# Optimization experiments

Hardware: AMD Instinct MI355X
Metric: run time of the kernel (lower is better)

Reference implementation:

```python
import jax, jax.numpy as jnp
import numpy as np

B, S, H = 1, 2048, 2048
NH, HD, RD = 32, 64, 64      # n_heads, head_dim, qk_mqa_dim (rope dim)
QR, KVR = 1024, 896          # q_lora_rank, kv_lora_rank
EPS = 1e-6
SCALE = HD ** -0.5           # scaling = head_dim ** -0.5 (as in module)


def rotate_half(x):
    x1, x2 = jnp.split(x, 2, axis=-1)
    return jnp.concatenate((-x2, x1), axis=-1)


def rmsnorm(x, w):
    var = jnp.mean(jnp.square(x), axis=-1, keepdims=True)
    return x * jax.lax.rsqrt(var + EPS) * w


def setup_inputs() -> dict:
    key = jax.random.key(0)
    ks = jax.random.split(key, 8)
    hidden_states = jax.random.normal(ks[0], (B, S, H), jnp.float32)
    # rotary tables over RD dims (applied only to the rope slice)
    inv_freq = 1.0 / (10000.0 ** (np.arange(0, RD, 2, dtype=np.float32) / RD))
    ang = np.arange(S, dtype=np.float32)[:, None] * inv_freq[None, :]
    emb = np.concatenate([ang, ang], axis=-1)  # [S, RD]
    cos = jnp.tile(jnp.asarray(np.cos(emb))[None], (B, 1, 1))
    sin = jnp.tile(jnp.asarray(np.sin(emb))[None], (B, 1, 1))
    s = 0.02
    q_a_w = s * jax.random.normal(ks[1], (QR, H), jnp.float32)
    q_a_ln_w = jnp.ones((QR,), jnp.float32)
    q_b_w = s * jax.random.normal(ks[2], (NH * (HD + RD), QR), jnp.float32)
    kv_a_w = s * jax.random.normal(ks[3], (KVR + RD, H), jnp.float32)
    kv_a_ln_w = jnp.ones((KVR,), jnp.float32)
    kv_b_w = s * jax.random.normal(ks[4], (NH * 2 * HD, KVR), jnp.float32)
    o_w = s * jax.random.normal(ks[5], (H, NH * HD), jnp.float32)
    return {"hidden_states": hidden_states, "cos": cos, "sin": sin,
            "q_a_w": q_a_w, "q_a_ln_w": q_a_ln_w, "q_b_w": q_b_w,
            "kv_a_w": kv_a_w, "kv_a_ln_w": kv_a_ln_w, "kv_b_w": kv_b_w,
            "o_w": o_w}


def reference(hidden_states, cos, sin, q_a_w, q_a_ln_w, q_b_w,
              kv_a_w, kv_a_ln_w, kv_b_w, o_w):
    b, s, _ = hidden_states.shape
    # Q: low-rank down -> RMSNorm -> up, split nope/rope per head
    q_lat = rmsnorm(hidden_states @ q_a_w.T, q_a_ln_w)             # [B,S,QR]
    q = (q_lat @ q_b_w.T).reshape(b, s, NH, HD + RD).transpose(0, 2, 1, 3)
    q_nope, q_rope = q[..., :HD], q[..., HD:]                      # [B,NH,S,HD/RD]
    # KV: joint down-proj with shared MQA rope key
    ckv = hidden_states @ kv_a_w.T                                 # [B,S,KVR+RD]
    c_kv, k_rope = ckv[..., :KVR], ckv[..., KVR:]
    k_rope = k_rope[:, None]                                       # [B,1,S,RD]
    kv = (rmsnorm(c_kv, kv_a_ln_w) @ kv_b_w.T).reshape(b, s, NH, 2 * HD)
    kv = kv.transpose(0, 2, 1, 3)                                  # [B,NH,S,2HD]
    k_nope, v = kv[..., :HD], kv[..., HD:]
    # RoPE on rope slices only (cos/sin unsqueezed over head dim)
    c_, s_ = cos[:, None], sin[:, None]
    q_rope = q_rope * c_ + rotate_half(q_rope) * s_
    k_rope = k_rope * c_ + rotate_half(k_rope) * s_
    q_full = jnp.concatenate([q_nope, q_rope], axis=-1)            # [B,NH,S,HD+RD]
    k_full = jnp.concatenate(
        [k_nope, jnp.broadcast_to(k_rope, (b, NH, s, RD))], axis=-1)
    # causal SDPA
    scores = jnp.einsum('bhqd,bhkd->bhqk', q_full, k_full) * SCALE
    mask = jnp.tril(jnp.ones((s, s), bool))
    scores = jnp.where(mask, scores, jnp.finfo(scores.dtype).min)
    attn = jax.nn.softmax(scores, axis=-1)
    out = jnp.einsum('bhqk,bhkd->bhqd', attn, v)                   # [B,NH,S,HD]
    out = out.transpose(0, 2, 1, 3).reshape(b, s, NH * HD)
    return out @ o_w.T                                             # [B,S,H]
```

## Files before the change

### kernel.cpp

```cpp
#include <hip/hip_runtime.h>


typedef __attribute__((ext_vector_type(8))) __bf16 bf16x8;
typedef __attribute__((ext_vector_type(4))) float f32x4;
typedef __attribute__((ext_vector_type(4))) unsigned u32x4;

__device__ __forceinline__ unsigned short f2bf(float f) {
  unsigned int x = __builtin_bit_cast(unsigned int, f);
  x += 0x7fffu + ((x >> 16) & 1u);
  return (unsigned short)(x >> 16);
}
__device__ __forceinline__ void gload_lds16(const void* g, void* l) {
  __builtin_amdgcn_global_load_lds(
      (const __attribute__((address_space(1))) void*)g,
      (__attribute__((address_space(3))) void*)l, 16, 0, 0);
}

struct CvtSegs {
  const float* src[6];
  unsigned short* dst[6];
  unsigned int n_src[6];
  unsigned int n_tot[6];
  unsigned int blk0[7];
};

__global__ __launch_bounds__(256) void cvt_all(CvtSegs sg) {
  int b = blockIdx.x;
  int seg = 0;
#pragma unroll
  for (int k = 0; k < 5; ++k)
    if (b >= (int)sg.blk0[k + 1]) seg = k + 1;
  size_t i = ((size_t)(b - sg.blk0[seg]) * 256 + threadIdx.x) * 4;
  if (i >= sg.n_tot[seg]) return;
  unsigned short o0 = 0, o1 = 0, o2 = 0, o3 = 0;
  if (i < sg.n_src[seg]) {
    float4 v = *reinterpret_cast<const float4*>(sg.src[seg] + i);
    o0 = f2bf(v.x); o1 = f2bf(v.y); o2 = f2bf(v.z); o3 = f2bf(v.w);
  }
  *reinterpret_cast<ushort4*>(sg.dst[seg] + i) = make_ushort4(o0, o1, o2, o3);
}

__global__ __launch_bounds__(512, 4) void gemm_bt2(const unsigned short* __restrict__ A,
                                                   const unsigned short* __restrict__ B,
                                                   float* __restrict__ C,
                                                   int M, int N, int K) {
  __shared__ unsigned short lA0[128 * 64], lA1[128 * 64];
  __shared__ unsigned short lB0[64 * 64], lB1[64 * 64];
  const int tid = threadIdx.x, lane = tid & 63, wv = tid >> 6;
  const int wr = wv >> 1, wc = wv & 1;
  const int bm = blockIdx.y * 128, bn = blockIdx.x * 64;

  f32x4 acc[2][2] = {};

  const int ar0 = tid >> 3;
  const int acol = (((tid & 7) ^ ((tid >> 3) & 7))) * 8;
  const int swz = lane & 7;

  auto stage = [&](unsigned short* la, unsigned short* lb, int k0) {
#pragma unroll
    for (int i = 0; i < 2; ++i)
      gload_lds16(A + (size_t)(bm + i * 64 + ar0) * K + k0 + acol,
                  &la[(i * 512 + wv * 64) * 8]);
    gload_lds16(B + (size_t)(bn + ar0) * K + k0 + acol, &lb[(wv * 64) * 8]);
  };

  auto compute = [&](const unsigned short* la, const unsigned short* lb) {
#pragma unroll
    for (int ks = 0; ks < 2; ++ks) {
      const int ch = ((ks * 4 + (lane >> 4)) ^ swz) * 8;
      bf16x8 af[2], bfr[2];
#pragma unroll
      for (int m = 0; m < 2; ++m)
        af[m] = *reinterpret_cast<const bf16x8*>(
            &la[(wr * 32 + m * 16 + (lane & 15)) * 64 + ch]);
#pragma unroll
      for (int n = 0; n < 2; ++n)
        bfr[n] = *reinterpret_cast<const bf16x8*>(
            &lb[(wc * 32 + n * 16 + (lane & 15)) * 64 + ch]);
      __builtin_amdgcn_s_setprio(1);
#pragma unroll
      for (int m = 0; m < 2; ++m)
#pragma unroll
        for (int n = 0; n < 2; ++n)
          acc[m][n] = __builtin_amdgcn_mfma_f32_16x16x32_bf16(af[m], bfr[n], acc[m][n], 0, 0, 0);
      __builtin_amdgcn_s_setprio(0);
    }
  };

  stage(lA0, lB0, 0);
  for (int k0 = 0; k0 < K; k0 += 128) {
    __syncthreads();
    stage(lA1, lB1, k0 + 64);
    compute(lA0, lB0);
    __syncthreads();
    if (k0 + 128 < K) stage(lA0, lB0, k0 + 128);
    compute(lA1, lB1);
  }

  const int r0 = bm + wr * 32, c0 = bn + wc * 32;
#pragma unroll
  for (int m = 0; m < 2; ++m)
#pragma unroll
    for (int n = 0; n < 2; ++n)
#pragma unroll
      for (int r = 0; r < 4; ++r)
        C[(size_t)(r0 + m * 16 + (lane >> 4) * 4 + r) * N + c0 + n * 16 + (lane & 15)] =
            acc[m][n][r];
}

__global__ __launch_bounds__(256) void rmsnorm_rope(const float* __restrict__ C1,
                                                    const float* __restrict__ qw,
                                                    const float* __restrict__ kvw,
                                                    const float* __restrict__ cosp,
                                                    const float* __restrict__ sinp,
                                                    unsigned short* __restrict__ qn,
                                                    unsigned short* __restrict__ ckvn,
                                                    unsigned short* __restrict__ kr) {
  const int s = blockIdx.x, tid = threadIdx.x;
  const float* row = C1 + (size_t)s * 2048;
  __shared__ float red[4];

  float4 v = *reinterpret_cast<const float4*>(row + tid * 4);
  float ss = v.x * v.x + v.y * v.y + v.z * v.z + v.w * v.w;
  ss += __shfl_xor(ss, 32); ss += __shfl_xor(ss, 16); ss += __shfl_xor(ss, 8);
  ss += __shfl_xor(ss, 4);  ss += __shfl_xor(ss, 2);  ss += __shfl_xor(ss, 1);
  if ((tid & 63) == 0) red[tid >> 6] = ss;
  __syncthreads();
  float rs = rsqrtf((red[0] + red[1] + red[2] + red[3]) * (1.f / 1024.f) + 1e-6f);
  {
    float4 w = *reinterpret_cast<const float4*>(qw + tid * 4);
    *reinterpret_cast<ushort4*>(qn + (size_t)s * 1024 + tid * 4) =
        make_ushort4(f2bf(v.x * rs * w.x), f2bf(v.y * rs * w.y),
                     f2bf(v.z * rs * w.z), f2bf(v.w * rs * w.w));
  }

  float4 u = make_float4(0.f, 0.f, 0.f, 0.f);
  if (tid < 224) u = *reinterpret_cast<const float4*>(row + 1024 + tid * 4);
  ss = u.x * u.x + u.y * u.y + u.z * u.z + u.w * u.w;
  ss += __shfl_xor(ss, 32); ss += __shfl_xor(ss, 16); ss += __shfl_xor(ss, 8);
  ss += __shfl_xor(ss, 4);  ss += __shfl_xor(ss, 2);  ss += __shfl_xor(ss, 1);
  __syncthreads();
  if ((tid & 63) == 0) red[tid >> 6] = ss;
  __syncthreads();
  rs = rsqrtf((red[0] + red[1] + red[2] + red[3]) * (1.f / 896.f) + 1e-6f);
  if (tid < 224) {
    float4 w = *reinterpret_cast<const float4*>(kvw + tid * 4);
    *reinterpret_cast<ushort4*>(ckvn + (size_t)s * 896 + tid * 4) =
        make_ushort4(f2bf(u.x * rs * w.x), f2bf(u.y * rs * w.y),
                     f2bf(u.z * rs * w.z), f2bf(u.w * rs * w.w));
  }

  if (tid < 64) {
    int d = tid;
    float x = row[1920 + d];
    float part = (d < 32) ? -row[1920 + d + 32] : row[1920 + d - 32];
    float vv = x * cosp[(size_t)s * 64 + d] + part * sinp[(size_t)s * 64 + d];
    kr[(size_t)s * 64 + d] = f2bf(vv);
  }
}

__global__ __launch_bounds__(256) void q_post(const float* __restrict__ Qf,
                                              const float* __restrict__ cosp,
                                              const float* __restrict__ sinp,
                                              unsigned short* __restrict__ Qb) {
  size_t base = ((size_t)blockIdx.x * 256 + threadIdx.x) * 4;
  int s = (int)(base >> 12);
  int w = (int)(base & 127);
  float4 x = *reinterpret_cast<const float4*>(Qf + base);
  float4 o;
  if (w < 64) {
    o = x;
  } else {
    int d = w - 64;
    float sgn = (d < 32) ? -1.f : 1.f;
    float4 prt = (d < 32) ? *reinterpret_cast<const float4*>(Qf + base + 32)
                          : *reinterpret_cast<const float4*>(Qf + base - 32);
    float4 c = *reinterpret_cast<const float4*>(cosp + (size_t)s * 64 + d);
    float4 sn = *reinterpret_cast<const float4*>(sinp + (size_t)s * 64 + d);
    o.x = x.x * c.x + sgn * prt.x * sn.x;
    o.y = x.y * c.y + sgn * prt.y * sn.y;
    o.z = x.z * c.z + sgn * prt.z * sn.z;
    o.w = x.w * c.w + sgn * prt.w * sn.w;
  }
  const float SC = 0.18033688f;
  *reinterpret_cast<ushort4*>(Qb + base) =
      make_ushort4(f2bf(o.x * SC), f2bf(o.y * SC), f2bf(o.z * SC), f2bf(o.w * SC));
}

__global__ __launch_bounds__(256) void kv_post(const float* __restrict__ KVf,
                                               const unsigned short* __restrict__ kr,
                                               unsigned short* __restrict__ Kb,
                                               unsigned short* __restrict__ Vt) {
  __shared__ float lT[64 * 65];
  const int s0 = blockIdx.x * 64, h = blockIdx.y, tid = threadIdx.x;
  for (int idx = tid; idx < 4096; idx += 256) {
    int r = idx >> 6, c = idx & 63;
    size_t base = (size_t)(s0 + r) * 4096 + h * 128;
    Kb[base + c] = f2bf(KVf[base + c]);
    Kb[base + 64 + c] = kr[(size_t)(s0 + r) * 64 + c];
    lT[r * 65 + c] = KVf[base + 64 + c];
  }
  __syncthreads();
  for (int idx = tid; idx < 4096; idx += 256) {
    int d = idx >> 6, c = idx & 63;
    Vt[((size_t)h * 64 + d) * 2048 + s0 + c] = f2bf(lT[c * 65 + d]);
  }
}

__global__ __launch_bounds__(256, 4) void flash_attn(const unsigned short* __restrict__ Qb,
                                                     const unsigned short* __restrict__ Kb,
                                                     const unsigned short* __restrict__ Vt,
                                                     float* __restrict__ Op,
                                                     float2* __restrict__ Ml) {
  __shared__ unsigned short lK0[64 * 128], lK1[64 * 128];
  const int tid = threadIdx.x, lane = tid & 63, wv = tid >> 6;
  const int h = blockIdx.x;
  const int qb = 31 - ((int)blockIdx.y >> 1);
  const int j = (int)blockIdx.y & 1;
  const int q0 = qb * 64;
  const int firstrow = q0 + wv * 16;
  const int qa = firstrow + (lane & 15);

  bf16x8 qf[4];
  {
    const unsigned short* qrow = Qb + (size_t)(firstrow + (lane & 15)) * 4096 + h * 128;
#pragma unroll
    for (int ks = 0; ks < 4; ++ks)
      qf[ks] = *reinterpret_cast<const bf16x8*>(qrow + ks * 32 + (lane >> 4) * 8);
  }

  f32x4 o_acc[4] = {};
  float mrow = -1e30f, lrow = 0.f;

  const int g = lane >> 4;
  const int sl0 = ((g & 1) * 2) * 16 + (lane & 15);
  const int sl1 = sl0 + 16;
  const bool hi = g >= 2;

  const int krow = wv * 4 + (lane >> 4);
  const int kcol = (((lane & 15) ^ (krow & 7)) * 8);
  const int swz = lane & 7;

  auto stage = [&](int t, unsigned short* lK) {
    int j0 = t * 64;
#pragma unroll
    for (int i = 0; i < 4; ++i)
      gload_lds16(Kb + (size_t)(j0 + i * 16 + krow) * 4096 + h * 128 + kcol,
                  &lK[(i * 16 + wv * 4) * 128]);
  };

  auto loadV = [&](int j0, bf16x8 (&vr)[2][4]) {
#pragma unroll
    for (int ks = 0; ks < 2; ++ks)
#pragma unroll
      for (int n = 0; n < 4; ++n)
        vr[ks][n] = *reinterpret_cast<const bf16x8*>(
            Vt + ((size_t)h * 64 + n * 16 + (lane & 15)) * 2048 + j0 + ks * 32 +
            (lane >> 4) * 8);
  };

  auto computeT = [&](int j0, const unsigned short* lK, const bf16x8 (&vr)[2][4]) {
    f32x4 sT[4] = {};
    __builtin_amdgcn_s_setprio(1);
#pragma unroll
    for (int n = 0; n < 4; ++n)
#pragma unroll
      for (int ks = 0; ks < 4; ++ks) {
        bf16x8 kf = *reinterpret_cast<const bf16x8*>(
            &lK[(n * 16 + (lane & 15)) * 128 + (((ks * 4 + (lane >> 4)) ^ swz)) * 8]);
        sT[n] = __builtin_amdgcn_mfma_f32_16x16x32_bf16(kf, qf[ks], sT[n], 0, 0, 0);
      }
    __builtin_amdgcn_s_setprio(0);

    if (j0 == q0) {
#pragma unroll
      for (int n = 0; n < 4; ++n)
#pragma unroll
        for (int r = 0; r < 4; ++r) {
          int key = j0 + n * 16 + g * 4 + r;
          if (key > qa) sT[n][r] = -1e30f;
        }
    }

    float mx = sT[0][0];
#pragma unroll
    for (int n = 0; n < 4; ++n)
#pragma unroll
      for (int r = 0; r < 4; ++r) mx = fmaxf(mx, sT[n][r]);
    mx = fmaxf(mx, __shfl_xor(mx, 16));
    mx = fmaxf(mx, __shfl_xor(mx, 32));

    if (__any(mx - mrow > 8.0f)) {
      float mn = fmaxf(mrow, mx);
      float sf = exp2f(mrow - mn);
      mrow = mn;
      lrow *= sf;
      float sfr[4];
#pragma unroll
      for (int r = 0; r < 4; ++r) sfr[r] = __shfl(sf, (lane >> 4) * 4 + r);
#pragma unroll
      for (int n = 0; n < 4; ++n)
#pragma unroll
        for (int r = 0; r < 4; ++r) o_acc[n][r] *= sfr[r];
    }

    float ps = 0.f;
    unsigned dw[4][2];
#pragma unroll
    for (int n = 0; n < 4; ++n) {
      float p0 = exp2f(sT[n][0] - mrow), p1 = exp2f(sT[n][1] - mrow);
      float p2 = exp2f(sT[n][2] - mrow), p3 = exp2f(sT[n][3] - mrow);
      ps += (p0 + p1) + (p2 + p3);
      asm("v_cvt_pk_bf16_f32 %0, %1, %2" : "=v"(dw[n][0]) : "v"(p0), "v"(p1));
      asm("v_cvt_pk_bf16_f32 %0, %1, %2" : "=v"(dw[n][1]) : "v"(p2), "v"(p3));
    }
    ps += __shfl_xor(ps, 16);
    ps += __shfl_xor(ps, 32);
    lrow += ps;

#pragma unroll
    for (int ks = 0; ks < 2; ++ks) {
      unsigned A0 = __shfl(dw[2 * ks][0], sl0);
      unsigned B0 = __shfl(dw[2 * ks + 1][0], sl0);
      unsigned A1 = __shfl(dw[2 * ks][1], sl0);
      unsigned B1 = __shfl(dw[2 * ks + 1][1], sl0);
      unsigned A2 = __shfl(dw[2 * ks][0], sl1);
      unsigned B2 = __shfl(dw[2 * ks + 1][0], sl1);
      unsigned A3 = __shfl(dw[2 * ks][1], sl1);
      unsigned B3 = __shfl(dw[2 * ks + 1][1], sl1);
      u32x4 mm;
      mm.x = hi ? B0 : A0; mm.y = hi ? B1 : A1;
      mm.z = hi ? B2 : A2; mm.w = hi ? B3 : A3;
      bf16x8 pa = __builtin_bit_cast(bf16x8, mm);
      __builtin_amdgcn_s_setprio(1);
#pragma unroll
      for (int n = 0; n < 4; ++n)
        o_acc[n] = __builtin_amdgcn_mfma_f32_16x16x32_bf16(pa, vr[ks][n], o_acc[n], 0, 0, 0);
      __builtin_amdgcn_s_setprio(0);
    }
  };

  bf16x8 vr[2][4];
  unsigned short* cur = lK0;
  unsigned short* nxt = lK1;
  if (j <= qb) stage(j, cur);
  for (int t = j; t <= qb; t += 2) {
    __syncthreads();
    if (t + 2 <= qb) stage(t + 2, nxt);
    loadV(t * 64, vr);
    computeT(t * 64, cur, vr);
    unsigned short* tmp = cur; cur = nxt; nxt = tmp;
  }

  float* op = Op + (size_t)j * 4194304 + ((size_t)h * 2048 + firstrow) * 64;
#pragma unroll
  for (int n = 0; n < 4; ++n)
#pragma unroll
    for (int r = 0; r < 4; ++r)
      op[(size_t)(g * 4 + r) * 64 + n * 16 + (lane & 15)] = o_acc[n][r];
  if (lane < 16)
    Ml[(size_t)j * 65536 + h * 2048 + qa] = make_float2(mrow, lrow);
}

__global__ __launch_bounds__(256) void flash_combine(const float* __restrict__ Op,
                                                     const float2* __restrict__ Ml,
                                                     unsigned short* __restrict__ Ao) {
  size_t i4 = ((size_t)blockIdx.x * 256 + threadIdx.x) * 4;
  int s = (int)(i4 >> 11);
  int c = (int)(i4 & 2047);
  int h = c >> 6, d = c & 63;
  float2 a = Ml[h * 2048 + s];
  float2 b = Ml[65536 + h * 2048 + s];
  float M = fmaxf(a.x, b.x);
  float w0 = exp2f(a.x - M), w1 = exp2f(b.x - M);
  float inv = 1.f / (w0 * a.y + w1 * b.y);
  size_t pidx = ((size_t)h * 2048 + s) * 64 + d;
  float4 o0 = *reinterpret_cast<const float4*>(Op + pidx);
  float4 o1 = *reinterpret_cast<const float4*>(Op + 4194304 + pidx);
  *reinterpret_cast<ushort4*>(Ao + (size_t)s * 2048 + h * 64 + d) =
      make_ushort4(f2bf((w0 * o0.x + w1 * o1.x) * inv),
                   f2bf((w0 * o0.y + w1 * o1.y) * inv),
                   f2bf((w0 * o0.z + w1 * o1.z) * inv),
                   f2bf((w0 * o0.w + w1 * o1.w) * inv));
}

extern "C" void kernel_launch(void* const* d_in, const int* in_sizes, int n_in,
                              void* d_out, int out_size, void* d_ws, size_t ws_size,
                              hipStream_t stream) {
  const float* hs   = (const float*)d_in[0];
  const float* cosp = (const float*)d_in[1];
  const float* sinp = (const float*)d_in[2];
  const float* qaw  = (const float*)d_in[3];
  const float* qaln = (const float*)d_in[4];
  const float* qbwf = (const float*)d_in[5];
  const float* kvaw = (const float*)d_in[6];
  const float* kvln = (const float*)d_in[7];
  const float* kvbwf= (const float*)d_in[8];
  const float* owf  = (const float*)d_in[9];
  float* out = (float*)d_out;
  char* ws = (char*)d_ws;
  const size_t MB = 1u << 20;

  unsigned short* W1b  = (unsigned short*)(ws + 0);
  unsigned short* Ao   = (unsigned short*)(ws + 0);
  unsigned short* qbw  = (unsigned short*)(ws + 8 * MB);
  unsigned short* Vt   = (unsigned short*)(ws + 8 * MB);
  unsigned short* kvbw = (unsigned short*)(ws + 16 * MB);
  unsigned short* owb  = (unsigned short*)(ws + 23 * MB);
  unsigned short* hsb  = (unsigned short*)(ws + 31 * MB);
  unsigned short* Qb   = (unsigned short*)(ws + 31 * MB);
  float*          C1   = (float*)(ws + 39 * MB);
  unsigned short* Kb   = (unsigned short*)(ws + 47 * MB);
  unsigned short* qln  = (unsigned short*)(ws + 55 * MB);
  unsigned short* ckvn = (unsigned short*)(ws + 59 * MB);
  unsigned short* kr   = (unsigned short*)(ws + 63 * MB);
  float*          Qf   = (float*)(ws + 64 * MB);
  float*          KVf  = (float*)(ws + 96 * MB);
  float*          Op   = (float*)(ws + 64 * MB);
  float2*         Mlp  = (float2*)(ws + 98 * MB);
  (void)ws_size; (void)in_sizes; (void)n_in; (void)out_size;

  CvtSegs sg;
  sg.src[0] = qaw;   sg.dst[0] = W1b;                      sg.n_src[0] = 1024u * 2048u; sg.n_tot[0] = 1024u * 2048u;
  sg.src[1] = kvaw;  sg.dst[1] = W1b + (size_t)1024 * 2048; sg.n_src[1] = 960u * 2048u;  sg.n_tot[1] = 1024u * 2048u;
  sg.src[2] = hs;    sg.dst[2] = hsb;                      sg.n_src[2] = 2048u * 2048u; sg.n_tot[2] = 2048u * 2048u;
  sg.src[3] = qbwf;  sg.dst[3] = qbw;                      sg.n_src[3] = 4096u * 1024u; sg.n_tot[3] = 4096u * 1024u;
  sg.src[4] = kvbwf; sg.dst[4] = kvbw;                     sg.n_src[4] = 4096u * 896u;  sg.n_tot[4] = 4096u * 896u;
  sg.src[5] = owf;   sg.dst[5] = owb;                      sg.n_src[5] = 2048u * 2048u; sg.n_tot[5] = 2048u * 2048u;
  sg.blk0[0] = 0;
  for (int k = 0; k < 6; ++k) sg.blk0[k + 1] = sg.blk0[k] + sg.n_tot[k] / 1024u;
  cvt_all<<<dim3(sg.blk0[6]), 256, 0, stream>>>(sg);

  gemm_bt2<<<dim3(32, 16), 512, 0, stream>>>(hsb, W1b, C1, 2048, 2048, 2048);
  rmsnorm_rope<<<2048, 256, 0, stream>>>(C1, qaln, kvln, cosp, sinp, qln, ckvn, kr);
  gemm_bt2<<<dim3(64, 16), 512, 0, stream>>>(qln, qbw, Qf, 2048, 4096, 1024);
  gemm_bt2<<<dim3(64, 16), 512, 0, stream>>>(ckvn, kvbw, KVf, 2048, 4096, 896);

  q_post<<<dim3((unsigned)(((size_t)2048 * 4096) / 1024)), 256, 0, stream>>>(Qf, cosp, sinp, Qb);
  kv_post<<<dim3(32, 32), 256, 0, stream>>>(KVf, kr, Kb, Vt);

  flash_attn<<<dim3(32, 64), 256, 0, stream>>>(Qb, Kb, Vt, Op, Mlp);
  flash_combine<<<dim3(4096), 256, 0, stream>>>(Op, Mlp, Ao);

  gemm_bt2<<<dim3(32, 16), 512, 0, stream>>>(Ao, owb, out, 2048, 2048, 2048);
}
```

Before: 223.3 us.

## Fuse Q RoPE/scale and K assembly into attention, emit bf16 GEMM outputs

The Q and KV up-projection GEMMs now write bf16 directly instead of fp32. The q_post kernel is removed: RoPE and the softmax scale are applied to Q inside flash_attn while fragments load. K tiles are staged straight from the KV GEMM output and the shared rope key buffer, which removes the separate Kb assembly. The GEMM also gets an XCD-aware workgroup index swizzle, and the softmax max/sum reductions are tree-shaped. The intent is to cut intermediate memory traffic and kernel launches. In exchange, Q is rounded to bf16 before RoPE, adding one extra rounding step.

```diff
diff --git a/kernel.cpp b/kernel.cpp
--- a/kernel.cpp
+++ b/kernel.cpp
@@ -10,11 +10,17 @@
   x += 0x7fffu + ((x >> 16) & 1u);
   return (unsigned short)(x >> 16);
 }
+__device__ __forceinline__ float bf2f(unsigned short u) {
+  unsigned int x = ((unsigned int)u) << 16;
+  return __builtin_bit_cast(float, x);
+}
 __device__ __forceinline__ void gload_lds16(const void* g, void* l) {
   __builtin_amdgcn_global_load_lds(
       (const __attribute__((address_space(1))) void*)g,
       (__attribute__((address_space(3))) void*)l, 16, 0, 0);
 }
+__device__ __forceinline__ void cstore(float* C, size_t i, float v) { C[i] = v; }
+__device__ __forceinline__ void cstore(unsigned short* C, size_t i, float v) { C[i] = f2bf(v); }
 
 struct CvtSegs {
   const float* src[6];
@@ -40,15 +46,21 @@
   *reinterpret_cast<ushort4*>(sg.dst[seg] + i) = make_ushort4(o0, o1, o2, o3);
 }
 
+template <typename OutT>
 __global__ __launch_bounds__(512, 4) void gemm_bt2(const unsigned short* __restrict__ A,
                                                    const unsigned short* __restrict__ B,
-                                                   float* __restrict__ C,
+                                                   OutT* __restrict__ C,
                                                    int M, int N, int K) {
   __shared__ unsigned short lA0[128 * 64], lA1[128 * 64];
   __shared__ unsigned short lB0[64 * 64], lB1[64 * 64];
   const int tid = threadIdx.x, lane = tid & 63, wv = tid >> 6;
   const int wr = wv >> 1, wc = wv & 1;
-  const int bm = blockIdx.y * 128, bn = blockIdx.x * 64;
+
+  unsigned nwg = gridDim.x * gridDim.y;
+  unsigned lid = blockIdx.y * gridDim.x + blockIdx.x;
+  unsigned swz_id = (lid & 7) * (nwg >> 3) + (lid >> 3);
+  const int bm = (int)(swz_id / gridDim.x) * 128;
+  const int bn = (int)(swz_id % gridDim.x) * 64;
 
   f32x4 acc[2][2] = {};
 
@@ -104,8 +116,8 @@
     for (int n = 0; n < 2; ++n)
 #pragma unroll
       for (int r = 0; r < 4; ++r)
-        C[(size_t)(r0 + m * 16 + (lane >> 4) * 4 + r) * N + c0 + n * 16 + (lane & 15)] =
-            acc[m][n][r];
+        cstore(C, (size_t)(r0 + m * 16 + (lane >> 4) * 4 + r) * N + c0 + n * 16 + (lane & 15),
+               acc[m][n][r]);
 }
 
 __global__ __launch_bounds__(256) void rmsnorm_rope(const float* __restrict__ C1,
@@ -159,56 +171,26 @@
   }
 }
 
-__global__ __launch_bounds__(256) void q_post(const float* __restrict__ Qf,
-                                              const float* __restrict__ cosp,
-                                              const float* __restrict__ sinp,
-                                              unsigned short* __restrict__ Qb) {
-  size_t base = ((size_t)blockIdx.x * 256 + threadIdx.x) * 4;
-  int s = (int)(base >> 12);
-  int w = (int)(base & 127);
-  float4 x = *reinterpret_cast<const float4*>(Qf + base);
-  float4 o;
-  if (w < 64) {
-    o = x;
-  } else {
-    int d = w - 64;
-    float sgn = (d < 32) ? -1.f : 1.f;
-    float4 prt = (d < 32) ? *reinterpret_cast<const float4*>(Qf + base + 32)
-                          : *reinterpret_cast<const float4*>(Qf + base - 32);
-    float4 c = *reinterpret_cast<const float4*>(cosp + (size_t)s * 64 + d);
-    float4 sn = *reinterpret_cast<const float4*>(sinp + (size_t)s * 64 + d);
-    o.x = x.x * c.x + sgn * prt.x * sn.x;
-    o.y = x.y * c.y + sgn * prt.y * sn.y;
-    o.z = x.z * c.z + sgn * prt.z * sn.z;
-    o.w = x.w * c.w + sgn * prt.w * sn.w;
-  }
-  const float SC = 0.18033688f;
-  *reinterpret_cast<ushort4*>(Qb + base) =
-      make_ushort4(f2bf(o.x * SC), f2bf(o.y * SC), f2bf(o.z * SC), f2bf(o.w * SC));
-}
-
-__global__ __launch_bounds__(256) void kv_post(const float* __restrict__ KVf,
-                                               const unsigned short* __restrict__ kr,
-                                               unsigned short* __restrict__ Kb,
+__global__ __launch_bounds__(256) void kv_post(const unsigned short* __restrict__ KVfb,
                                                unsigned short* __restrict__ Vt) {
-  __shared__ float lT[64 * 65];
+  __shared__ unsigned short lT[64 * 65];
   const int s0 = blockIdx.x * 64, h = blockIdx.y, tid = threadIdx.x;
   for (int idx = tid; idx < 4096; idx += 256) {
     int r = idx >> 6, c = idx & 63;
-    size_t base = (size_t)(s0 + r) * 4096 + h * 128;
-    Kb[base + c] = f2bf(KVf[base + c]);
-    Kb[base + 64 + c] = kr[(size_t)(s0 + r) * 64 + c];
-    lT[r * 65 + c] = KVf[base + 64 + c];
+    lT[r * 65 + c] = KVfb[(size_t)(s0 + r) * 4096 + h * 128 + 64 + c];
   }
   __syncthreads();
   for (int idx = tid; idx < 4096; idx += 256) {
     int d = idx >> 6, c = idx & 63;
-    Vt[((size_t)h * 64 + d) * 2048 + s0 + c] = f2bf(lT[c * 65 + d]);
-  }
-}
-
-__global__ __launch_bounds__(256, 4) void flash_attn(const unsigned short* __restrict__ Qb,
-                                                     const unsigned short* __restrict__ Kb,
+    Vt[((size_t)h * 64 + d) * 2048 + s0 + c] = lT[c * 65 + d];
+  }
+}
+
+__global__ __launch_bounds__(256, 4) void flash_attn(const unsigned short* __restrict__ Qfb,
+                                                     const unsigned short* __restrict__ KVfb,
+                                                     const unsigned short* __restrict__ kr,
+                                                     const float* __restrict__ cosp,
+                                                     const float* __restrict__ sinp,
                                                      const unsigned short* __restrict__ Vt,
                                                      float* __restrict__ Op,
                                                      float2* __restrict__ Ml) {
@@ -219,34 +201,74 @@
   const int j = (int)blockIdx.y & 1;
   const int q0 = qb * 64;
   const int firstrow = q0 + wv * 16;
+  const int g = lane >> 4;
   const int qa = firstrow + (lane & 15);
+  const float SC = 0.18033688f;
 
   bf16x8 qf[4];
   {
-    const unsigned short* qrow = Qb + (size_t)(firstrow + (lane & 15)) * 4096 + h * 128;
+    const unsigned short* qr = Qfb + (size_t)qa * 4096 + h * 128;
+    float raw[4][8];
+#pragma unroll
+    for (int ks = 0; ks < 4; ++ks) {
+      ushort4 u0 = *reinterpret_cast<const ushort4*>(qr + ks * 32 + g * 8);
+      ushort4 u1 = *reinterpret_cast<const ushort4*>(qr + ks * 32 + g * 8 + 4);
+      raw[ks][0] = bf2f(u0.x); raw[ks][1] = bf2f(u0.y);
+      raw[ks][2] = bf2f(u0.z); raw[ks][3] = bf2f(u0.w);
+      raw[ks][4] = bf2f(u1.x); raw[ks][5] = bf2f(u1.y);
+      raw[ks][6] = bf2f(u1.z); raw[ks][7] = bf2f(u1.w);
+    }
+    const float* cp = cosp + (size_t)qa * 64 + g * 8;
+    const float* sp = sinp + (size_t)qa * 64 + g * 8;
+    float c0[8], s0[8], c1[8], s1[8];
+    {
+      float4 a = *reinterpret_cast<const float4*>(cp);
+      float4 b = *reinterpret_cast<const float4*>(cp + 4);
+      c0[0]=a.x;c0[1]=a.y;c0[2]=a.z;c0[3]=a.w;c0[4]=b.x;c0[5]=b.y;c0[6]=b.z;c0[7]=b.w;
+      a = *reinterpret_cast<const float4*>(cp + 32);
+      b = *reinterpret_cast<const float4*>(cp + 36);
+      c1[0]=a.x;c1[1]=a.y;c1[2]=a.z;c1[3]=a.w;c1[4]=b.x;c1[5]=b.y;c1[6]=b.z;c1[7]=b.w;
+      a = *reinterpret_cast<const float4*>(sp);
+      b = *reinterpret_cast<const float4*>(sp + 4);
+      s0[0]=a.x;s0[1]=a.y;s0[2]=a.z;s0[3]=a.w;s0[4]=b.x;s0[5]=b.y;s0[6]=b.z;s0[7]=b.w;
+      a = *reinterpret_cast<const float4*>(sp + 32);
+      b = *reinterpret_cast<const float4*>(sp + 36);
+      s1[0]=a.x;s1[1]=a.y;s1[2]=a.z;s1[3]=a.w;s1[4]=b.x;s1[5]=b.y;s1[6]=b.z;s1[7]=b.w;
+    }
+    alignas(16) unsigned short pk[4][8];
+#pragma unroll
+    for (int e = 0; e < 8; ++e) {
+      pk[0][e] = f2bf(raw[0][e] * SC);
+      pk[1][e] = f2bf(raw[1][e] * SC);
+      pk[2][e] = f2bf((raw[2][e] * c0[e] - raw[3][e] * s0[e]) * SC);
+      pk[3][e] = f2bf((raw[3][e] * c1[e] + raw[2][e] * s1[e]) * SC);
+    }
 #pragma unroll
     for (int ks = 0; ks < 4; ++ks)
-      qf[ks] = *reinterpret_cast<const bf16x8*>(qrow + ks * 32 + (lane >> 4) * 8);
+      qf[ks] = *reinterpret_cast<const bf16x8*>(pk[ks]);
   }
 
   f32x4 o_acc[4] = {};
   float mrow = -1e30f, lrow = 0.f;
 
-  const int g = lane >> 4;
   const int sl0 = ((g & 1) * 2) * 16 + (lane & 15);
   const int sl1 = sl0 + 16;
   const bool hi = g >= 2;
 
   const int krow = wv * 4 + (lane >> 4);
-  const int kcol = (((lane & 15) ^ (krow & 7)) * 8);
+  const int cs = (lane & 15) ^ (krow & 7);
   const int swz = lane & 7;
 
   auto stage = [&](int t, unsigned short* lK) {
-    int j0 = t * 64;
-#pragma unroll
-    for (int i = 0; i < 4; ++i)
-      gload_lds16(Kb + (size_t)(j0 + i * 16 + krow) * 4096 + h * 128 + kcol,
-                  &lK[(i * 16 + wv * 4) * 128]);
+    int jj = t * 64;
+#pragma unroll
+    for (int i = 0; i < 4; ++i) {
+      int s = jj + i * 16 + krow;
+      const unsigned short* src =
+          (cs < 8) ? KVfb + (size_t)s * 4096 + h * 128 + cs * 8
+                   : kr + (size_t)s * 64 + (cs - 8) * 8;
+      gload_lds16(src, &lK[(i * 16 + wv * 4) * 128]);
+    }
   };
 
   auto loadV = [&](int j0, bf16x8 (&vr)[2][4]) {
@@ -282,11 +304,11 @@
         }
     }
 
-    float mx = sT[0][0];
+    float tm[4];
 #pragma unroll
     for (int n = 0; n < 4; ++n)
-#pragma unroll
-      for (int r = 0; r < 4; ++r) mx = fmaxf(mx, sT[n][r]);
+      tm[n] = fmaxf(fmaxf(sT[n][0], sT[n][1]), fmaxf(sT[n][2], sT[n][3]));
+    float mx = fmaxf(fmaxf(tm[0], tm[1]), fmaxf(tm[2], tm[3]));
     mx = fmaxf(mx, __shfl_xor(mx, 16));
     mx = fmaxf(mx, __shfl_xor(mx, 32));
 
@@ -304,16 +326,17 @@
         for (int r = 0; r < 4; ++r) o_acc[n][r] *= sfr[r];
     }
 
-    float ps = 0.f;
+    float psn[4];
     unsigned dw[4][2];
 #pragma unroll
     for (int n = 0; n < 4; ++n) {
       float p0 = exp2f(sT[n][0] - mrow), p1 = exp2f(sT[n][1] - mrow);
       float p2 = exp2f(sT[n][2] - mrow), p3 = exp2f(sT[n][3] - mrow);
-      ps += (p0 + p1) + (p2 + p3);
+      psn[n] = (p0 + p1) + (p2 + p3);
       asm("v_cvt_pk_bf16_f32 %0, %1, %2" : "=v"(dw[n][0]) : "v"(p0), "v"(p1));
       asm("v_cvt_pk_bf16_f32 %0, %1, %2" : "=v"(dw[n][1]) : "v"(p2), "v"(p3));
     }
+    float ps = (psn[0] + psn[1]) + (psn[2] + psn[3]);
     ps += __shfl_xor(ps, 16);
     ps += __shfl_xor(ps, 32);
     lrow += ps;
@@ -408,16 +431,14 @@
   unsigned short* kvbw = (unsigned short*)(ws + 16 * MB);
   unsigned short* owb  = (unsigned short*)(ws + 23 * MB);
   unsigned short* hsb  = (unsigned short*)(ws + 31 * MB);
-  unsigned short* Qb   = (unsigned short*)(ws + 31 * MB);
-  float*          C1   = (float*)(ws + 39 * MB);
-  unsigned short* Kb   = (unsigned short*)(ws + 47 * MB);
-  unsigned short* qln  = (unsigned short*)(ws + 55 * MB);
-  unsigned short* ckvn = (unsigned short*)(ws + 59 * MB);
-  unsigned short* kr   = (unsigned short*)(ws + 63 * MB);
-  float*          Qf   = (float*)(ws + 64 * MB);
-  float*          KVf  = (float*)(ws + 96 * MB);
-  float*          Op   = (float*)(ws + 64 * MB);
-  float2*         Mlp  = (float2*)(ws + 98 * MB);
+  unsigned short* Qfb  = (unsigned short*)(ws + 31 * MB);
+  float*          C1   = (float*)(ws + 47 * MB);
+  unsigned short* KVfb = (unsigned short*)(ws + 63 * MB);
+  unsigned short* kr   = (unsigned short*)(ws + 79 * MB);
+  unsigned short* qln  = (unsigned short*)(ws + 80 * MB);
+  unsigned short* ckvn = (unsigned short*)(ws + 84 * MB);
+  float*          Op   = (float*)(ws + 88 * MB);
+  float2*         Mlp  = (float2*)(ws + 122 * MB);
   (void)ws_size; (void)in_sizes; (void)n_in; (void)out_size;
 
   CvtSegs sg;
@@ -431,16 +452,15 @@
   for (int k = 0; k < 6; ++k) sg.blk0[k + 1] = sg.blk0[k] + sg.n_tot[k] / 1024u;
   cvt_all<<<dim3(sg.blk0[6]), 256, 0, stream>>>(sg);
 
-  gemm_bt2<<<dim3(32, 16), 512, 0, stream>>>(hsb, W1b, C1, 2048, 2048, 2048);
+  gemm_bt2<float><<<dim3(32, 16), 512, 0, stream>>>(hsb, W1b, C1, 2048, 2048, 2048);
   rmsnorm_rope<<<2048, 256, 0, stream>>>(C1, qaln, kvln, cosp, sinp, qln, ckvn, kr);
-  gemm_bt2<<<dim3(64, 16), 512, 0, stream>>>(qln, qbw, Qf, 2048, 4096, 1024);
-  gemm_bt2<<<dim3(64, 16), 512, 0, stream>>>(ckvn, kvbw, KVf, 2048, 4096, 896);
-
-  q_post<<<dim3((unsigned)(((size_t)2048 * 4096) / 1024)), 256, 0, stream>>>(Qf, cosp, sinp, Qb);
-  kv_post<<<dim3(32, 32), 256, 0, stream>>>(KVf, kr, Kb, Vt);
-
-  flash_attn<<<dim3(32, 64), 256, 0, stream>>>(Qb, Kb, Vt, Op, Mlp);
+  gemm_bt2<unsigned short><<<dim3(64, 16), 512, 0, stream>>>(qln, qbw, Qfb, 2048, 4096, 1024);
+  gemm_bt2<unsigned short><<<dim3(64, 16), 512, 0, stream>>>(ckvn, kvbw, KVfb, 2048, 4096, 896);
+
+  kv_post<<<dim3(32, 32), 256, 0, stream>>>(KVfb, Vt);
+
+  flash_attn<<<dim3(32, 64), 256, 0, stream>>>(Qfb, KVfb, kr, cosp, sinp, Vt, Op, Mlp);
   flash_combine<<<dim3(4096), 256, 0, stream>>>(Op, Mlp, Ao);
 
-  gemm_bt2<<<dim3(32, 16), 512, 0, stream>>>(Ao, owb, out, 2048, 2048, 2048);
-}
+  gemm_bt2<float><<<dim3(32, 16), 512, 0, stream>>>(Ao, owb, out, 2048, 2048, 2048);
+}
```

New measurement: 221.0 us. No clear change (-1.0%).
